# Kernel tuning notes

Hardware: AMD Instinct MI355X
Metric: run time of the kernel (lower is better)

Reference implementation:

```python
import jax, jax.numpy as jnp
import numpy as np

B, SQ, SK, D, DV = 2, 1024, 1024, 64, 64
NEG = -1e9


def setup_inputs() -> dict:
    key = jax.random.key(0)
    kq, kk, kv, km = jax.random.split(key, 4)
    return {
        "q": jax.random.normal(kq, (B, SQ, D), dtype=jnp.float32),
        "k": jax.random.normal(kk, (B, SK, D), dtype=jnp.float32),
        "v": jax.random.normal(kv, (B, SK, DV), dtype=jnp.float32),
        "mask": jax.random.randint(km, (B, SK), 0, 2, dtype=jnp.int32),
    }


def reference(q, k, v, mask):
    # L1 (Manhattan) distance scores: [B, Sq, Sk]
    dist = jnp.sum(jnp.abs(q[:, :, None, :] - k[:, None, :, :]), axis=-1)
    scores = -dist
    # mask: [B, Sk] -> broadcast over queries as [B, 1, Sk]
    scores = jnp.where(mask[:, None, :] == 0, NEG, scores)
    attention = jax.nn.softmax(scores, axis=-1)
    # weighted sum of values: [B, Sq, Dv]
    return jnp.einsum("bqk,bkd->bqd", attention, v)
```

## Files before the change

kernel.cpp:

```cpp
#include <hip/hip_runtime.h>
#include <math.h>

#define B_ 2
#define SQ_ 1024
#define SK_ 1024
#define D_ 64
#define DV_ 64
#define QB 4
#define TPB 256
#define NEGC (-1e9f)

__global__ __launch_bounds__(TPB) void manh_attn_kernel(
    const float* __restrict__ qg, const float* __restrict__ kg,
    const float* __restrict__ vg, const int* __restrict__ maskg,
    float* __restrict__ outg) {
  __shared__ float qs[QB * D_];
  __shared__ float p[QB][SK_];
  __shared__ float pv[16][QB][DV_];
  __shared__ float redm[4][QB];
  __shared__ float redl[4][QB];

  const int tid = threadIdx.x;
  const int b = blockIdx.x / (SQ_ / QB);
  const int q0 = (blockIdx.x % (SQ_ / QB)) * QB;

  qs[tid] = qg[((size_t)b * SQ_ + q0) * D_ + tid];
  __syncthreads();

  const float* kb = kg + (size_t)b * SK_ * D_;
  const int* mb = maskg + (size_t)b * SK_;

  float sreg[4][QB];
  float lmax[QB];
#pragma unroll
  for (int qq = 0; qq < QB; ++qq) lmax[qq] = -INFINITY;

#pragma unroll
  for (int j = 0; j < 4; ++j) {
    const int kk = tid + 256 * j;
    const float4* kr = (const float4*)(kb + (size_t)kk * D_);
    float dist[QB];
#pragma unroll
    for (int qq = 0; qq < QB; ++qq) dist[qq] = 0.f;
#pragma unroll
    for (int i = 0; i < 16; ++i) {
      float4 k4 = kr[i];
#pragma unroll
      for (int qq = 0; qq < QB; ++qq) {
        float4 q4 = ((const float4*)qs)[qq * 16 + i];
        dist[qq] += fabsf(q4.x - k4.x) + fabsf(q4.y - k4.y) +
                    fabsf(q4.z - k4.z) + fabsf(q4.w - k4.w);
      }
    }
    const int mk = mb[kk];
#pragma unroll
    for (int qq = 0; qq < QB; ++qq) {
      float s = (mk == 0) ? NEGC : -dist[qq];
      sreg[j][qq] = s;
      lmax[qq] = fmaxf(lmax[qq], s);
    }
  }

#pragma unroll
  for (int off = 32; off > 0; off >>= 1) {
#pragma unroll
    for (int qq = 0; qq < QB; ++qq)
      lmax[qq] = fmaxf(lmax[qq], __shfl_down(lmax[qq], off, 64));
  }
  if ((tid & 63) == 0) {
#pragma unroll
    for (int qq = 0; qq < QB; ++qq) redm[tid >> 6][qq] = lmax[qq];
  }
  __syncthreads();
  float m[QB];
#pragma unroll
  for (int qq = 0; qq < QB; ++qq)
    m[qq] = fmaxf(fmaxf(redm[0][qq], redm[1][qq]),
                  fmaxf(redm[2][qq], redm[3][qq]));

  float lsum[QB];
#pragma unroll
  for (int qq = 0; qq < QB; ++qq) lsum[qq] = 0.f;
#pragma unroll
  for (int j = 0; j < 4; ++j) {
    const int kk = tid + 256 * j;
#pragma unroll
    for (int qq = 0; qq < QB; ++qq) {
      float e = __expf(sreg[j][qq] - m[qq]);
      p[qq][kk] = e;
      lsum[qq] += e;
    }
  }
#pragma unroll
  for (int off = 32; off > 0; off >>= 1) {
#pragma unroll
    for (int qq = 0; qq < QB; ++qq)
      lsum[qq] += __shfl_down(lsum[qq], off, 64);
  }
  if ((tid & 63) == 0) {
#pragma unroll
    for (int qq = 0; qq < QB; ++qq) redl[tid >> 6][qq] = lsum[qq];
  }
  __syncthreads();

  const int col = tid & 15;
  const int chunk = tid >> 4;
  const float* vb = vg + (size_t)b * SK_ * DV_;
  float4 acc[QB];
#pragma unroll
  for (int qq = 0; qq < QB; ++qq) acc[qq] = make_float4(0.f, 0.f, 0.f, 0.f);

#pragma unroll 8
  for (int t = 0; t < 64; ++t) {
    const int kk = chunk * 64 + t;
    float4 v4 = ((const float4*)(vb + (size_t)kk * DV_))[col];
#pragma unroll
    for (int qq = 0; qq < QB; ++qq) {
      float pw = p[qq][kk];
      acc[qq].x += pw * v4.x;
      acc[qq].y += pw * v4.y;
      acc[qq].z += pw * v4.z;
      acc[qq].w += pw * v4.w;
    }
  }
#pragma unroll
  for (int qq = 0; qq < QB; ++qq)
    ((float4*)&pv[chunk][qq][0])[col] = acc[qq];
  __syncthreads();

  const int qq2 = tid >> 6;
  const int d2 = tid & 63;
  float s = 0.f;
#pragma unroll
  for (int c = 0; c < 16; ++c) s += pv[c][qq2][d2];
  const float linv =
      1.f / (redl[0][qq2] + redl[1][qq2] + redl[2][qq2] + redl[3][qq2]);
  outg[((size_t)b * SQ_ + q0 + qq2) * DV_ + d2] = s * linv;
}

extern "C" void kernel_launch(void* const* d_in, const int* in_sizes, int n_in,
                              void* d_out, int out_size, void* d_ws,
                              size_t ws_size, hipStream_t stream) {
  const float* q = (const float*)d_in[0];
  const float* k = (const float*)d_in[1];
  const float* v = (const float*)d_in[2];
  const int* mask = (const int*)d_in[3];
  float* out = (float*)d_out;
  dim3 grid(B_ * (SQ_ / QB));
  manh_attn_kernel<<<grid, TPB, 0, stream>>>(q, k, v, mask, out);
}
```

Baseline: 90.72 us.

## Interleave K loads across rows, pack probabilities as float4, reorder PV access

Restructures the distance loop so each thread loads four K rows per feature step, reusing the query registers across them and exposing more memory-level parallelism. Probabilities are stored as one float4 per key (all four queries together), so the PV loop reads a single vector from shared memory. The PV loop now interleaves key chunks across thread groups, which changes V access locality. It also adds a launch-bounds occupancy hint, at the cost of higher register pressure from the 16 distance accumulators.

New measurement: 85.48 us. -5.8%, faster.

```diff
diff --git a/kernel.cpp b/kernel.cpp
--- a/kernel.cpp
+++ b/kernel.cpp
@@ -10,67 +10,74 @@
 #define TPB 256
 #define NEGC (-1e9f)
 
-__global__ __launch_bounds__(TPB) void manh_attn_kernel(
+__global__ __launch_bounds__(TPB, 4) void manh_attn_kernel(
     const float* __restrict__ qg, const float* __restrict__ kg,
     const float* __restrict__ vg, const int* __restrict__ maskg,
     float* __restrict__ outg) {
-  __shared__ float qs[QB * D_];
-  __shared__ float p[QB][SK_];
+  __shared__ float4 qs4[QB * 16];
+  __shared__ float4 p4[SK_];
   __shared__ float pv[16][QB][DV_];
   __shared__ float redm[4][QB];
   __shared__ float redl[4][QB];
 
   const int tid = threadIdx.x;
-  const int b = blockIdx.x / (SQ_ / QB);
-  const int q0 = (blockIdx.x % (SQ_ / QB)) * QB;
+  const int b = blockIdx.x >> 8;
+  const int q0 = (blockIdx.x & 255) * QB;
 
-  qs[tid] = qg[((size_t)b * SQ_ + q0) * D_ + tid];
+  ((float*)qs4)[tid] = qg[((size_t)b * SQ_ + q0) * D_ + tid];
   __syncthreads();
 
-  const float* kb = kg + (size_t)b * SK_ * D_;
+  const float4* kb4 = (const float4*)(kg + (size_t)b * SK_ * D_);
   const int* mb = maskg + (size_t)b * SK_;
 
-  float sreg[4][QB];
+  int mk[4];
+#pragma unroll
+  for (int j = 0; j < 4; ++j) mk[j] = mb[tid + 256 * j];
+
+  float dist[4][QB];
+#pragma unroll
+  for (int j = 0; j < 4; ++j)
+#pragma unroll
+    for (int qq = 0; qq < QB; ++qq) dist[j][qq] = 0.f;
+
+#pragma unroll 4
+  for (int i = 0; i < 16; ++i) {
+    float4 k4[4];
+#pragma unroll
+    for (int j = 0; j < 4; ++j) k4[j] = kb4[(size_t)(tid + 256 * j) * 16 + i];
+    float4 q4[QB];
+#pragma unroll
+    for (int qq = 0; qq < QB; ++qq) q4[qq] = qs4[qq * 16 + i];
+#pragma unroll
+    for (int j = 0; j < 4; ++j) {
+#pragma unroll
+      for (int qq = 0; qq < QB; ++qq) {
+        dist[j][qq] += fabsf(q4[qq].x - k4[j].x) + fabsf(q4[qq].y - k4[j].y) +
+                       fabsf(q4[qq].z - k4[j].z) + fabsf(q4[qq].w - k4[j].w);
+      }
+    }
+  }
+
   float lmax[QB];
 #pragma unroll
   for (int qq = 0; qq < QB; ++qq) lmax[qq] = -INFINITY;
-
 #pragma unroll
   for (int j = 0; j < 4; ++j) {
-    const int kk = tid + 256 * j;
-    const float4* kr = (const float4*)(kb + (size_t)kk * D_);
-    float dist[QB];
-#pragma unroll
-    for (int qq = 0; qq < QB; ++qq) dist[qq] = 0.f;
-#pragma unroll
-    for (int i = 0; i < 16; ++i) {
-      float4 k4 = kr[i];
-#pragma unroll
-      for (int qq = 0; qq < QB; ++qq) {
-        float4 q4 = ((const float4*)qs)[qq * 16 + i];
-        dist[qq] += fabsf(q4.x - k4.x) + fabsf(q4.y - k4.y) +
-                    fabsf(q4.z - k4.z) + fabsf(q4.w - k4.w);
-      }
-    }
-    const int mk = mb[kk];
 #pragma unroll
     for (int qq = 0; qq < QB; ++qq) {
-      float s = (mk == 0) ? NEGC : -dist[qq];
-      sreg[j][qq] = s;
+      float s = (mk[j] == 0) ? NEGC : -dist[j][qq];
+      dist[j][qq] = s;
       lmax[qq] = fmaxf(lmax[qq], s);
     }
   }
-
 #pragma unroll
-  for (int off = 32; off > 0; off >>= 1) {
+  for (int off = 32; off > 0; off >>= 1)
 #pragma unroll
     for (int qq = 0; qq < QB; ++qq)
       lmax[qq] = fmaxf(lmax[qq], __shfl_down(lmax[qq], off, 64));
-  }
-  if ((tid & 63) == 0) {
+  if ((tid & 63) == 0)
 #pragma unroll
     for (int qq = 0; qq < QB; ++qq) redm[tid >> 6][qq] = lmax[qq];
-  }
   __syncthreads();
   float m[QB];
 #pragma unroll
@@ -83,45 +90,43 @@
   for (int qq = 0; qq < QB; ++qq) lsum[qq] = 0.f;
 #pragma unroll
   for (int j = 0; j < 4; ++j) {
-    const int kk = tid + 256 * j;
+    float e[QB];
 #pragma unroll
     for (int qq = 0; qq < QB; ++qq) {
-      float e = __expf(sreg[j][qq] - m[qq]);
-      p[qq][kk] = e;
-      lsum[qq] += e;
+      e[qq] = __expf(dist[j][qq] - m[qq]);
+      lsum[qq] += e[qq];
     }
+    p4[tid + 256 * j] = make_float4(e[0], e[1], e[2], e[3]);
   }
 #pragma unroll
-  for (int off = 32; off > 0; off >>= 1) {
+  for (int off = 32; off > 0; off >>= 1)
 #pragma unroll
-    for (int qq = 0; qq < QB; ++qq)
-      lsum[qq] += __shfl_down(lsum[qq], off, 64);
-  }
-  if ((tid & 63) == 0) {
+    for (int qq = 0; qq < QB; ++qq) lsum[qq] += __shfl_down(lsum[qq], off, 64);
+  if ((tid & 63) == 0)
 #pragma unroll
     for (int qq = 0; qq < QB; ++qq) redl[tid >> 6][qq] = lsum[qq];
-  }
   __syncthreads();
 
   const int col = tid & 15;
   const int chunk = tid >> 4;
-  const float* vb = vg + (size_t)b * SK_ * DV_;
+  const float4* vb4 = (const float4*)(vg + (size_t)b * SK_ * DV_);
   float4 acc[QB];
 #pragma unroll
   for (int qq = 0; qq < QB; ++qq) acc[qq] = make_float4(0.f, 0.f, 0.f, 0.f);
 
-#pragma unroll 8
+#pragma unroll 4
   for (int t = 0; t < 64; ++t) {
-    const int kk = chunk * 64 + t;
-    float4 v4 = ((const float4*)(vb + (size_t)kk * DV_))[col];
-#pragma unroll
-    for (int qq = 0; qq < QB; ++qq) {
-      float pw = p[qq][kk];
-      acc[qq].x += pw * v4.x;
-      acc[qq].y += pw * v4.y;
-      acc[qq].z += pw * v4.z;
-      acc[qq].w += pw * v4.w;
-    }
+    const int kk = t * 16 + chunk;
+    float4 v4 = vb4[(size_t)kk * 16 + col];
+    float4 pw = p4[kk];
+    acc[0].x += pw.x * v4.x; acc[0].y += pw.x * v4.y;
+    acc[0].z += pw.x * v4.z; acc[0].w += pw.x * v4.w;
+    acc[1].x += pw.y * v4.x; acc[1].y += pw.y * v4.y;
+    acc[1].z += pw.y * v4.z; acc[1].w += pw.y * v4.w;
+    acc[2].x += pw.z * v4.x; acc[2].y += pw.z * v4.y;
+    acc[2].z += pw.z * v4.z; acc[2].w += pw.z * v4.w;
+    acc[3].x += pw.w * v4.x; acc[3].y += pw.w * v4.y;
+    acc[3].z += pw.w * v4.z; acc[3].w += pw.w * v4.w;
   }
 #pragma unroll
   for (int qq = 0; qq < QB; ++qq)
```
